# Optimization experiments

Measured on AMD Instinct MI355X. Metric: run time of the kernel, lower is better.

## Reference

```python
import math
import jax, jax.numpy as jnp
import numpy as np

B, C, H, W = 64, 1536, 16, 16
M_CLUSTERS, L_DIM, G_DIM, HID = 64, 128, 256, 512


def setup_inputs() -> dict:
    key = jax.random.key(0)
    ks = jax.random.split(key, 10)

    def w(k, out_d, in_d):
        return jax.random.normal(k, (out_d, in_d), jnp.float32) * (1.0 / np.sqrt(in_d))

    return {
        "x": jax.random.normal(ks[0], (B, C, H, W), jnp.float32),
        "t": jax.random.normal(ks[1], (B, C), jnp.float32),
        # token_features: Linear(C,512) -> ReLU -> Linear(512, token_dim)
        "Wt1": w(ks[2], HID, C), "bt1": jnp.zeros((HID,), jnp.float32),
        "Wt2": w(ks[3], G_DIM, HID), "bt2": jnp.zeros((G_DIM,), jnp.float32),
        # cluster_features: Conv1x1(C,512) -> ReLU -> Conv1x1(512, cluster_dim)
        "Wc1": w(ks[4], HID, C), "bc1": jnp.zeros((HID,), jnp.float32),
        "Wc2": w(ks[5], L_DIM, HID), "bc2": jnp.zeros((L_DIM,), jnp.float32),
        # score: Conv1x1(C,512) -> ReLU -> Conv1x1(512, num_clusters)
        "Ws1": w(ks[6], HID, C), "bs1": jnp.zeros((HID,), jnp.float32),
        "Ws2": w(ks[7], M_CLUSTERS, HID), "bs2": jnp.zeros((M_CLUSTERS,), jnp.float32),
        "dust_bin": jnp.float32(1.0),
    }


def _l2norm(a, axis):
    n = jnp.maximum(jnp.linalg.norm(a, axis=axis, keepdims=True), 1e-12)
    return a / n


def _conv1x1_mlp(xf, W1, b1, W2, b2):
    # xf: [B, C, N]; 1x1 convs are channel GEMMs
    h = jax.nn.relu(jnp.einsum('oc,bcn->bon', W1, xf) + b1[None, :, None])
    return jnp.einsum('oc,bcn->bon', W2, h) + b2[None, :, None]


def _matching_probs(S, dust_bin, num_iters=3):
    # Sinkhorn with dustbin row (log domain), reg = 1.0
    b, m, n = S.shape
    dust_row = jnp.broadcast_to(dust_bin.astype(S.dtype), (b, 1, n))
    Ms = jnp.concatenate([S, dust_row], axis=1)  # [B, m+1, n]
    norm = -math.log(n + m)
    log_a = jnp.full((m + 1,), norm, S.dtype).at[-1].add(math.log(n - m))
    log_b = jnp.full((n,), norm, S.dtype)
    u = jnp.zeros((b, m + 1), S.dtype)
    v = jnp.zeros((b, n), S.dtype)
    for _ in range(num_iters):
        u = log_a[None, :] - jax.scipy.special.logsumexp(Ms + v[:, None, :], axis=2)
        v = log_b[None, :] - jax.scipy.special.logsumexp(Ms + u[:, :, None], axis=1)
    return Ms + u[:, :, None] + v[:, None, :] - norm  # log_P - norm


def reference(x, t, Wt1, bt1, Wt2, bt2, Wc1, bc1, Wc2, bc2, Ws1, bs1, Ws2, bs2, dust_bin):
    b, c, h, w = x.shape
    n = h * w
    xf = x.reshape(b, c, n)
    f = _conv1x1_mlp(xf, Wc1, bc1, Wc2, bc2)      # [B, l, N]
    s = _conv1x1_mlp(xf, Ws1, bs1, Ws2, bs2)      # [B, m, N]
    tok = jax.nn.relu(t @ Wt1.T + bt1) @ Wt2.T + bt2  # [B, g]

    log_p = _matching_probs(s, dust_bin, num_iters=3)
    p = jnp.exp(log_p)[:, :-1, :]                 # drop dustbin row -> [B, m, N]

    # (f.unsqueeze(2) * p.unsqueeze(1)).sum(-1) is exactly a batched matmul
    vlad = jnp.einsum('bln,bmn->blm', f, p)       # [B, l, m]
    vlad = _l2norm(vlad, axis=1).reshape(b, -1)   # intra-norm over l, then flatten(1)

    out = jnp.concatenate([_l2norm(tok, axis=-1), vlad], axis=-1)
    return _l2norm(out, axis=-1)
```

## Files before the change

kernel.cpp:

```cpp
#include <hip/hip_runtime.h>
#include <math.h>

#define BNT 16384

using f32x4 = __attribute__((ext_vector_type(4))) float;
using s16x8 = __attribute__((ext_vector_type(8))) short;

__device__ __forceinline__ unsigned short f32_to_bf16_rne(float f) {
  unsigned int u = __float_as_uint(f);
  u += 0x7FFFu + ((u >> 16) & 1u);
  return (unsigned short)(u >> 16);
}
__device__ __forceinline__ unsigned pack_bf16x2(float a, float b) {
  return (unsigned)f32_to_bf16_rne(a) | ((unsigned)f32_to_bf16_rne(b) << 16);
}

__device__ __forceinline__ void gload_lds16(const ushort* g, ushort* lds) {
  __builtin_amdgcn_global_load_lds(
      (const __attribute__((address_space(1))) unsigned int*)g,
      (__attribute__((address_space(3))) unsigned int*)lds, 16, 0, 0);
}

__global__ __launch_bounds__(256) void prep_all(
    const float* __restrict__ t, const float* __restrict__ Wt1,
    const float* __restrict__ Wt2, const float* __restrict__ Wc1,
    const float* __restrict__ Ws1, const float* __restrict__ bc1,
    const float* __restrict__ bs1, const float* __restrict__ Wc2,
    const float* __restrict__ Ws2, const float* __restrict__ bc2,
    const float* __restrict__ bs2, ushort* __restrict__ Tb,
    ushort* __restrict__ Wt1b, ushort* __restrict__ Wt2b,
    ushort* __restrict__ Wc1b, ushort* __restrict__ Ws1b,
    float* __restrict__ b1, ushort* __restrict__ A2, float* __restrict__ b2) {
  const int bid = blockIdx.x, tid = threadIdx.x;
  const float* src = nullptr;
  ushort* dst = nullptr;
  int i = 0;
  if (bid < 96) {
    src = t; dst = Tb; i = bid * 256 + tid;
  } else if (bid < 864) {
    src = Wt1; dst = Wt1b; i = (bid - 96) * 256 + tid;
  } else if (bid < 992) {
    src = Wt2; dst = Wt2b; i = (bid - 864) * 256 + tid;
  } else if (bid < 1760) {
    src = Wc1; dst = Wc1b; i = (bid - 992) * 256 + tid;
  } else if (bid < 2528) {
    src = Ws1; dst = Ws1b; i = (bid - 1760) * 256 + tid;
  } else if (bid < 2532) {
    const int j = (bid - 2528) * 256 + tid;
    b1[j] = j < 512 ? bc1[j] : bs1[j - 512];
    return;
  } else {
    const int r = bid - 2532;
    const int c = tid * 4;
    float v[4] = {0.f, 0.f, 0.f, 0.f};
    if (r < 128) {
      if (c < 512) {
#pragma unroll
        for (int j = 0; j < 4; ++j) v[j] = Wc2[r * 512 + c + j];
      }
    } else if (r < 192) {
      if (c >= 512) {
#pragma unroll
        for (int j = 0; j < 4; ++j) v[j] = Ws2[(r - 128) * 512 + (c - 512) + j];
      }
    }
    uint2 o;
    o.x = pack_bf16x2(v[0], v[1]);
    o.y = pack_bf16x2(v[2], v[3]);
    *(uint2*)(A2 + r * 1024 + c) = o;
    if (tid == 0) b2[r] = r < 128 ? bc2[r] : (r < 192 ? bs2[r - 128] : 0.f);
    return;
  }
  const float4 v = ((const float4*)src)[i];
  uint2 o;
  o.x = pack_bf16x2(v.x, v.y);
  o.y = pack_bf16x2(v.z, v.w);
  ((uint2*)dst)[i] = o;
}

__global__ __launch_bounds__(256) void token1_mfma(
    const ushort* __restrict__ Tb, const ushort* __restrict__ Wt1b,
    float* __restrict__ Pt) {
  const int ct = blockIdx.x, kc = blockIdx.y;
  const int tid = threadIdx.x, l = tid & 63, wv = tid >> 6;
  const int lr = l & 15, ko = l >> 4;
  const int col = ct * 64 + wv * 16 + lr;
  f32x4 acc[4];
#pragma unroll
  for (int r = 0; r < 4; ++r) acc[r] = (f32x4){0.f, 0.f, 0.f, 0.f};
  const int k0 = kc * 384;
#pragma unroll 4
  for (int ks = 0; ks < 12; ++ks) {
    const int k = k0 + ks * 32 + ko * 8;
    const s16x8 bf = *(const s16x8*)(Wt1b + (size_t)col * 1536 + k);
#pragma unroll
    for (int rf = 0; rf < 4; ++rf) {
      const s16x8 af = *(const s16x8*)(Tb + (size_t)(rf * 16 + lr) * 1536 + k);
      acc[rf] =
          __builtin_amdgcn_mfma_f32_16x16x32_bf16(af, bf, acc[rf], 0, 0, 0);
    }
  }
#pragma unroll
  for (int rf = 0; rf < 4; ++rf)
#pragma unroll
    for (int j = 0; j < 4; ++j) {
      const int row = rf * 16 + ko * 4 + j;
      Pt[((kc * 64 + row) << 9) + col] = acc[rf][j];
    }
}

__global__ __launch_bounds__(256) void token1_reduce(
    const float* __restrict__ Pt, const float* __restrict__ bt1,
    ushort* __restrict__ Hb) {
  const int i = blockIdx.x * 256 + threadIdx.x;
  const int row = i >> 8, c2 = (i & 255) * 2;
  float v0 = bt1[c2], v1 = bt1[c2 + 1];
#pragma unroll
  for (int kc = 0; kc < 4; ++kc) {
    v0 += Pt[((kc * 64 + row) << 9) + c2];
    v1 += Pt[((kc * 64 + row) << 9) + c2 + 1];
  }
  v0 = fmaxf(v0, 0.f);
  v1 = fmaxf(v1, 0.f);
  ((unsigned*)Hb)[i] = pack_bf16x2(v0, v1);
}

__global__ __launch_bounds__(256) void token2_mfma(
    const ushort* __restrict__ Hb, const ushort* __restrict__ Wt2b,
    const float* __restrict__ bt2, float* __restrict__ TK) {
  const int ct = blockIdx.x;
  const int tid = threadIdx.x, l = tid & 63, wv = tid >> 6;
  const int lr = l & 15, ko = l >> 4;
  const int col = ct * 64 + wv * 16 + lr;
  f32x4 acc[4];
#pragma unroll
  for (int r = 0; r < 4; ++r) acc[r] = (f32x4){0.f, 0.f, 0.f, 0.f};
#pragma unroll 4
  for (int ks = 0; ks < 16; ++ks) {
    const int k = ks * 32 + ko * 8;
    const s16x8 bf = *(const s16x8*)(Wt2b + (size_t)col * 512 + k);
#pragma unroll
    for (int rf = 0; rf < 4; ++rf) {
      const s16x8 af = *(const s16x8*)(Hb + (size_t)(rf * 16 + lr) * 512 + k);
      acc[rf] =
          __builtin_amdgcn_mfma_f32_16x16x32_bf16(af, bf, acc[rf], 0, 0, 0);
    }
  }
  const float bb = bt2[col];
#pragma unroll
  for (int rf = 0; rf < 4; ++rf)
#pragma unroll
    for (int j = 0; j < 4; ++j)
      TK[(rf * 16 + ko * 4 + j) * 256 + col] = acc[rf][j] + bb;
}

__global__ __launch_bounds__(256) void transpose_x_bf16(
    const float* __restrict__ x, ushort* __restrict__ XT) {
  __shared__ ushort lds[16384];
  const int cc = blockIdx.x * 64, b = blockIdx.y;
  const int t = threadIdx.x;
  const float* xb = x + b * 393216 + cc * 256;
#pragma unroll
  for (int i = 0; i < 16; ++i) {
    const int c0 = i * 4;
    const float v0 = xb[(c0 + 0) * 256 + t];
    const float v1 = xb[(c0 + 1) * 256 + t];
    const float v2 = xb[(c0 + 2) * 256 + t];
    const float v3 = xb[(c0 + 3) * 256 + t];
    uint2 o;
    o.x = pack_bf16x2(v0, v1);
    o.y = pack_bf16x2(v2, v3);
    const int g = c0 >> 3;
    const int waddr = t * 128 + (((g ^ (t & 7)) << 4) | ((c0 & 7) << 1));
    *(uint2*)((char*)lds + waddr) = o;
  }
  __syncthreads();
#pragma unroll
  for (int r = 0; r < 8; ++r) {
    const int j = r * 32 + (t >> 3), q = t & 7;
    const uint4 o =
        *(const uint4*)((const char*)lds + j * 128 + ((q ^ (j & 7)) << 4));
    *(uint4*)(XT + (size_t)(b * 256 + j) * 1536 + cc + q * 8) = o;
  }
}

__global__ __launch_bounds__(512) void gemm1_8ph(
    const ushort* __restrict__ A1, const ushort* __restrict__ Bt,
    const float* __restrict__ b1, ushort* __restrict__ HT) {
  __shared__ ushort lds[65536];
  const int tid = threadIdx.x, l = tid & 63, w = tid >> 6;
  const int bid = blockIdx.x;
  const int newid = (bid & 7) * 32 + (bid >> 3);
  const int m0 = (newid & 3) * 256, n0 = (newid >> 2) * 256;
  const int wr = w >> 2, wc = w & 3;
  const int lr = l & 15, kq = l >> 4;
  const int permK8 = (kq ^ ((lr >> 1) & 3)) * 8;
  const int aRow = wr * 128 + lr;
  const int bRow = wc * 64 + lr;

  f32x4 acc[8][4];
#pragma unroll
  for (int mi = 0; mi < 8; ++mi)
#pragma unroll
    for (int ni = 0; ni < 4; ++ni) acc[mi][ni] = (f32x4){0.f, 0.f, 0.f, 0.f};

  const int srow = tid >> 2, ssp = tid & 3;
  const int skq = ssp ^ ((srow >> 1) & 3);
  const ushort* sA0 = A1 + (size_t)(m0 + srow) * 1536 + skq * 8;
  const ushort* sA1 = A1 + (size_t)(m0 + srow + 128) * 1536 + skq * 8;
  const ushort* sB0 = Bt + (size_t)(n0 + srow) * 1536 + skq * 8;
  const ushort* sB1 = Bt + (size_t)(n0 + srow + 128) * 1536 + skq * 8;
  const int wofs = w * 512;

#define STG_A(tau, kh)                                              \
  do {                                                              \
    ushort* d = &lds[((((tau)&1) * 2 + (kh)) * 8192) + wofs];       \
    gload_lds16(sA0 + (tau)*64 + (kh)*32, d);                       \
    gload_lds16(sA1 + (tau)*64 + (kh)*32, d + 4096);                \
  } while (0)
#define STG_B(tau, kh)                                              \
  do {                                                              \
    ushort* d = &lds[32768 + ((((tau)&1) * 2 + (kh)) * 8192) + wofs]; \
    gload_lds16(sB0 + (tau)*64 + (kh)*32, d);                       \
    gload_lds16(sB1 + (tau)*64 + (kh)*32, d + 4096);                \
  } while (0)

  STG_A(0, 0);
  STG_B(0, 0);
  STG_A(0, 1);
  STG_B(0, 1);
  asm volatile("s_waitcnt vmcnt(0)" ::: "memory");
  __builtin_amdgcn_s_barrier();

  for (int sg = 0; sg < 24; ++sg) {
    const int rho = sg & 1;
    const int As0 = (rho * 2 + 0) * 8192, As1 = (rho * 2 + 1) * 8192;
    const int Bs0 = 32768 + As0, Bs1 = 32768 + As1;
    const bool st = (sg + 1) < 24;
    s16x8 af[4], bfv[4];

#pragma unroll
    for (int i = 0; i < 4; ++i)
      af[i] = *(const s16x8*)&lds[As0 + (aRow + i * 16) * 32 + permK8];
#pragma unroll
    for (int ni = 0; ni < 4; ++ni)
      bfv[ni] = *(const s16x8*)&lds[Bs0 + (bRow + ni * 16) * 32 + permK8];
    if (st) STG_A(sg + 1, 0);
    __builtin_amdgcn_s_barrier();
    __builtin_amdgcn_s_setprio(1);
#pragma unroll
    for (int i = 0; i < 4; ++i)
#pragma unroll
      for (int ni = 0; ni < 4; ++ni)
        acc[i][ni] = __builtin_amdgcn_mfma_f32_16x16x32_bf16(af[i], bfv[ni],
                                                             acc[i][ni], 0, 0, 0);
    __builtin_amdgcn_s_setprio(0);
    __builtin_amdgcn_s_barrier();

#pragma unroll
    for (int i = 0; i < 4; ++i)
      af[i] = *(const s16x8*)&lds[As0 + (aRow + 64 + i * 16) * 32 + permK8];
    if (st) STG_B(sg + 1, 0);
    if (sg < 23)
      asm volatile("s_waitcnt vmcnt(4)" ::: "memory");
    else
      asm volatile("s_waitcnt vmcnt(0)" ::: "memory");
    __builtin_amdgcn_s_barrier();
    __builtin_amdgcn_s_setprio(1);
#pragma unroll
    for (int i = 0; i < 4; ++i)
#pragma unroll
      for (int ni = 0; ni < 4; ++ni)
        acc[4 + i][ni] = __builtin_amdgcn_mfma_f32_16x16x32_bf16(
            af[i], bfv[ni], acc[4 + i][ni], 0, 0, 0);
    __builtin_amdgcn_s_setprio(0);
    __builtin_amdgcn_s_barrier();

#pragma unroll
    for (int i = 0; i < 4; ++i)
      af[i] = *(const s16x8*)&lds[As1 + (aRow + i * 16) * 32 + permK8];
#pragma unroll
    for (int ni = 0; ni < 4; ++ni)
      bfv[ni] = *(const s16x8*)&lds[Bs1 + (bRow + ni * 16) * 32 + permK8];
    if (st) STG_A(sg + 1, 1);
    __builtin_amdgcn_s_barrier();
    __builtin_amdgcn_s_setprio(1);
#pragma unroll
    for (int i = 0; i < 4; ++i)
#pragma unroll
      for (int ni = 0; ni < 4; ++ni)
        acc[i][ni] = __builtin_amdgcn_mfma_f32_16x16x32_bf16(af[i], bfv[ni],
                                                             acc[i][ni], 0, 0, 0);
    __builtin_amdgcn_s_setprio(0);
    __builtin_amdgcn_s_barrier();

#pragma unroll
    for (int i = 0; i < 4; ++i)
      af[i] = *(const s16x8*)&lds[As1 + (aRow + 64 + i * 16) * 32 + permK8];
    if (st) STG_B(sg + 1, 1);
    asm volatile("s_waitcnt vmcnt(4)" ::: "memory");
    __builtin_amdgcn_s_barrier();
    __builtin_amdgcn_s_setprio(1);
#pragma unroll
    for (int i = 0; i < 4; ++i)
#pragma unroll
      for (int ni = 0; ni < 4; ++ni)
        acc[4 + i][ni] = __builtin_amdgcn_mfma_f32_16x16x32_bf16(
            af[i], bfv[ni], acc[4 + i][ni], 0, 0, 0);
    __builtin_amdgcn_s_setprio(0);
    __builtin_amdgcn_s_barrier();
  }
#undef STG_A
#undef STG_B

#pragma unroll
  for (int mi = 0; mi < 8; ++mi) {
    const int rbase = m0 + wr * 128 + mi * 16 + kq * 4;
    float b4[4];
#pragma unroll
    for (int j = 0; j < 4; ++j) b4[j] = b1[rbase + j];
#pragma unroll
    for (int ni = 0; ni < 4; ++ni) {
      const int col = n0 + wc * 64 + ni * 16 + lr;
      const float v0 = fmaxf(acc[mi][ni][0] + b4[0], 0.f);
      const float v1 = fmaxf(acc[mi][ni][1] + b4[1], 0.f);
      const float v2 = fmaxf(acc[mi][ni][2] + b4[2], 0.f);
      const float v3 = fmaxf(acc[mi][ni][3] + b4[3], 0.f);
      uint2 o;
      o.x = pack_bf16x2(v0, v1);
      o.y = pack_bf16x2(v2, v3);
      *(uint2*)(HT + (size_t)col * 1024 + rbase) = o;
    }
  }
}

__global__ __launch_bounds__(256) void gemm2_mfma(
    const ushort* __restrict__ A2, const ushort* __restrict__ HT,
    const float* __restrict__ b2, float* __restrict__ C2,
    ushort* __restrict__ Fb) {
  constexpr int K = 1024;
  __shared__ ushort As[2 * 128 * 32];
  __shared__ ushort Bs[2 * 128 * 32];
  const int tid = threadIdx.x;
  const int l = tid & 63, w = tid >> 6;
  const int bid = blockIdx.x;
  const int newid = (bid & 7) * 32 + (bid >> 3);
  const int m0 = (newid & 1) * 128, n0 = (newid >> 1) * 128;
  const int wr = w >> 1, wc = w & 1;
  const int lr = l & 15, kq = l >> 4;

  f32x4 acc[4][4];
#pragma unroll
  for (int mi = 0; mi < 4; ++mi)
#pragma unroll
    for (int ni = 0; ni < 4; ++ni) acc[mi][ni] = (f32x4){0.f, 0.f, 0.f, 0.f};

  const int rA0 = tid >> 2;
  const int q8 = (tid & 3) * 8;
  ushort* AsW0 = As + (w * 64) * 8;
  ushort* AsW1 = As + (256 + w * 64) * 8;
  ushort* BsW0 = Bs + (w * 64) * 8;
  ushort* BsW1 = Bs + (256 + w * 64) * 8;
  const ushort* Arow0 = A2 + (size_t)(m0 + rA0) * K + q8;
  const ushort* Arow1 = A2 + (size_t)(m0 + rA0 + 64) * K + q8;
  const ushort* Brow0 = HT + (size_t)(n0 + rA0) * K + q8;
  const ushort* Brow1 = HT + (size_t)(n0 + rA0 + 64) * K + q8;

  gload_lds16(Arow0, AsW0);
  gload_lds16(Arow1, AsW1);
  gload_lds16(Brow0, BsW0);
  gload_lds16(Brow1, BsW1);
  __syncthreads();

  int cur = 0;
  for (int k0 = 0; k0 < K; k0 += 32) {
    const int nxt = cur ^ 1;
    if (k0 + 32 < K) {
      gload_lds16(Arow0 + k0 + 32, AsW0 + nxt * 4096);
      gload_lds16(Arow1 + k0 + 32, AsW1 + nxt * 4096);
      gload_lds16(Brow0 + k0 + 32, BsW0 + nxt * 4096);
      gload_lds16(Brow1 + k0 + 32, BsW1 + nxt * 4096);
    }
    const ushort* Ab = As + cur * 4096;
    const ushort* Bb = Bs + cur * 4096;
    s16x8 af[4], bfr[4];
#pragma unroll
    for (int mi = 0; mi < 4; ++mi)
      af[mi] = *(const s16x8*)(Ab + (wr * 64 + mi * 16 + lr) * 32 + kq * 8);
#pragma unroll
    for (int ni = 0; ni < 4; ++ni)
      bfr[ni] = *(const s16x8*)(Bb + (wc * 64 + ni * 16 + lr) * 32 + kq * 8);
#pragma unroll
    for (int mi = 0; mi < 4; ++mi)
#pragma unroll
      for (int ni = 0; ni < 4; ++ni)
        acc[mi][ni] = __builtin_amdgcn_mfma_f32_16x16x32_bf16(
            af[mi], bfr[ni], acc[mi][ni], 0, 0, 0);
    __syncthreads();
    cur = nxt;
  }

#pragma unroll
  for (int mi = 0; mi < 4; ++mi) {
    const int rbase = m0 + wr * 64 + mi * 16 + kq * 4;
    if (rbase < 192) {
      float b4[4];
#pragma unroll
      for (int j = 0; j < 4; ++j) b4[j] = b2[rbase + j];
      if (rbase < 128) {
#pragma unroll
        for (int ni = 0; ni < 4; ++ni) {
          const int col = n0 + wc * 64 + ni * 16 + lr;
#pragma unroll
          for (int j = 0; j < 4; ++j)
            Fb[(size_t)(rbase + j) * BNT + col] =
                f32_to_bf16_rne(acc[mi][ni][j] + b4[j]);
        }
      } else {
#pragma unroll
        for (int ni = 0; ni < 4; ++ni) {
          const int col = n0 + wc * 64 + ni * 16 + lr;
          float* cr = C2 + (size_t)rbase * BNT + col;
#pragma unroll
          for (int j = 0; j < 4; ++j)
            cr[(size_t)j * BNT] = acc[mi][ni][j] + b4[j];
        }
      }
    }
  }
}

__global__ __launch_bounds__(256) void sinkhorn_lin(
    const float* __restrict__ S, const float* __restrict__ dustp,
    ushort* __restrict__ Pb) {
  const int b = blockIdx.x, tid = threadIdx.x;
  const int lane = tid & 63, wave = tid >> 6;
  __shared__ float E[65][256];
  __shared__ float U[65];
  __shared__ float V[256];
  for (int idx = tid; idx < 16384; idx += 256) {
    const int m = idx >> 8, n = idx & 255;
    E[m][n] = expf(S[m * BNT + b * 256 + n]);
  }
  E[64][tid] = expf(dustp[0]);
  V[tid] = 1.f;
  const float Ai = 1.f / 320.f;
  const float Adust = 192.f / 320.f;
  const float Bn = 1.f / 320.f;
  __syncthreads();
  for (int it = 0; it < 3; ++it) {
    for (int i = wave; i < 65; i += 4) {
      float s = E[i][lane] * V[lane];
      s = fmaf(E[i][lane + 64], V[lane + 64], s);
      s = fmaf(E[i][lane + 128], V[lane + 128], s);
      s = fmaf(E[i][lane + 192], V[lane + 192], s);
#pragma unroll
      for (int off = 32; off; off >>= 1) s += __shfl_xor(s, off);
      if (lane == 0) U[i] = (i == 64 ? Adust : Ai) / s;
    }
    __syncthreads();
    {
      const int n = tid;
      float s = 0.f;
#pragma unroll 13
      for (int i = 0; i < 65; ++i) s = fmaf(E[i][n], U[i], s);
      V[n] = Bn / s;
    }
    __syncthreads();
  }
  for (int idx = tid; idx < 16384; idx += 256) {
    const int m = idx >> 8, n = idx & 255;
    Pb[b * 16384 + idx] = f32_to_bf16_rne(E[m][n] * U[m] * V[n] * 320.f);
  }
}

__global__ __launch_bounds__(256) void vlad_mfma(const ushort* __restrict__ Fb,
                                                 const ushort* __restrict__ Pb,
                                                 float* __restrict__ VL) {
  const int b = blockIdx.x;
  const int tid = threadIdx.x, l = tid & 63, w = tid >> 6;
  const int lr = l & 15, ko = l >> 4;
  f32x4 acc[2][4];
#pragma unroll
  for (int li = 0; li < 2; ++li)
#pragma unroll
    for (int ni = 0; ni < 4; ++ni) acc[li][ni] = (f32x4){0.f, 0.f, 0.f, 0.f};
  const ushort* Fbase = Fb + b * 256;
  const ushort* Pbase = Pb + b * 16384;
#pragma unroll
  for (int ks = 0; ks < 8; ++ks) {
    const int k = ks * 32 + ko * 8;
    s16x8 bfr[4];
#pragma unroll
    for (int ni = 0; ni < 4; ++ni)
      bfr[ni] = *(const s16x8*)(Pbase + (ni * 16 + lr) * 256 + k);
#pragma unroll
    for (int li = 0; li < 2; ++li) {
      const s16x8 af =
          *(const s16x8*)(Fbase + (size_t)(w * 32 + li * 16 + lr) * BNT + k);
#pragma unroll
      for (int ni = 0; ni < 4; ++ni)
        acc[li][ni] = __builtin_amdgcn_mfma_f32_16x16x32_bf16(
            af, bfr[ni], acc[li][ni], 0, 0, 0);
    }
  }
#pragma unroll
  for (int li = 0; li < 2; ++li)
#pragma unroll
    for (int ni = 0; ni < 4; ++ni)
#pragma unroll
      for (int j = 0; j < 4; ++j) {
        const int ll = w * 32 + li * 16 + ko * 4 + j;
        const int m = ni * 16 + lr;
        VL[b * 8192 + ll * 64 + m] = acc[li][ni][j];
      }
}

__global__ __launch_bounds__(256) void finalize_kernel(
    const float* __restrict__ TK, const float* __restrict__ VL,
    float* __restrict__ out) {
  const int b = blockIdx.x, tid = threadIdx.x;
  const int lane = tid & 63, wave = tid >> 6;
  __shared__ float sred[4];
  __shared__ float ssm_part[4][64];
  __shared__ float invm_s[64];
  __shared__ float totals[1];
  const float* vl = &VL[b * 8192];
  float accv = 0.f;
  for (int k = 0; k < 32; ++k) {
    const float xv = vl[tid + 256 * k];
    accv = fmaf(xv, xv, accv);
  }
  ssm_part[wave][lane] = accv;
  const float tv = TK[b * 256 + tid];
  float ss = tv * tv;
#pragma unroll
  for (int off = 32; off; off >>= 1) ss += __shfl_down(ss, off);
  if (lane == 0) sred[wave] = ss;
  __syncthreads();
  const float sstok = sred[0] + sred[1] + sred[2] + sred[3];
  const float invtok = 1.f / fmaxf(sqrtf(sstok), 1e-12f);
  float tpart = 0.f;
  if (wave == 0) {
    const float s4 = ssm_part[0][tid] + ssm_part[1][tid] + ssm_part[2][tid] +
                     ssm_part[3][tid];
    const float inv = 1.f / fmaxf(sqrtf(s4), 1e-12f);
    invm_s[tid] = inv;
    tpart = s4 * inv * inv;
#pragma unroll
    for (int off = 32; off; off >>= 1) tpart += __shfl_down(tpart, off);
    if (lane == 0) totals[0] = tpart;
  }
  __syncthreads();
  const float total = totals[0] + sstok * invtok * invtok;
  const float invT = 1.f / fmaxf(sqrtf(total), 1e-12f);
  float* ob = &out[b * 8448];
  ob[tid] = tv * invtok * invT;
  for (int k = 0; k < 32; ++k) {
    const int idx = tid + 256 * k;
    ob[256 + idx] = vl[idx] * invm_s[idx & 63] * invT;
  }
}

template <bool RELU>
__global__ __launch_bounds__(256) void gemm_tt(
    const float* __restrict__ A, const float* __restrict__ Bw,
    const float* __restrict__ bias, float* __restrict__ C, int K, int Nn) {
  __shared__ float As[16][68];
  __shared__ float Bs[16][68];
  const int tid = threadIdx.x;
  const int tx = tid & 15, ty = tid >> 4;
  const int n0 = blockIdx.x * 64;
  const int lrow = tid >> 2, lkq = (tid & 3) << 2;
  float acc[4][4];
#pragma unroll
  for (int r = 0; r < 4; ++r)
#pragma unroll
    for (int c = 0; c < 4; ++c) acc[r][c] = 0.f;
  for (int k0 = 0; k0 < K; k0 += 16) {
    const float4 av = *(const float4*)&A[lrow * K + k0 + lkq];
    const float4 bv = *(const float4*)&Bw[(n0 + lrow) * K + k0 + lkq];
    As[lkq + 0][lrow] = av.x;
    As[lkq + 1][lrow] = av.y;
    As[lkq + 2][lrow] = av.z;
    As[lkq + 3][lrow] = av.w;
    Bs[lkq + 0][lrow] = bv.x;
    Bs[lkq + 1][lrow] = bv.y;
    Bs[lkq + 2][lrow] = bv.z;
    Bs[lkq + 3][lrow] = bv.w;
    __syncthreads();
#pragma unroll
    for (int kk = 0; kk < 16; ++kk) {
      const float4 a4 = *(const float4*)&As[kk][ty << 2];
      const float4 b4 = *(const float4*)&Bs[kk][tx << 2];
      acc[0][0] = fmaf(a4.x, b4.x, acc[0][0]);
      acc[0][1] = fmaf(a4.x, b4.y, acc[0][1]);
      acc[0][2] = fmaf(a4.x, b4.z, acc[0][2]);
      acc[0][3] = fmaf(a4.x, b4.w, acc[0][3]);
      acc[1][0] = fmaf(a4.y, b4.x, acc[1][0]);
      acc[1][1] = fmaf(a4.y, b4.y, acc[1][1]);
      acc[1][2] = fmaf(a4.y, b4.z, acc[1][2]);
      acc[1][3] = fmaf(a4.y, b4.w, acc[1][3]);
      acc[2][0] = fmaf(a4.z, b4.x, acc[2][0]);
      acc[2][1] = fmaf(a4.z, b4.y, acc[2][1]);
      acc[2][2] = fmaf(a4.z, b4.z, acc[2][2]);
      acc[2][3] = fmaf(a4.z, b4.w, acc[2][3]);
      acc[3][0] = fmaf(a4.w, b4.x, acc[3][0]);
      acc[3][1] = fmaf(a4.w, b4.y, acc[3][1]);
      acc[3][2] = fmaf(a4.w, b4.z, acc[3][2]);
      acc[3][3] = fmaf(a4.w, b4.w, acc[3][3]);
    }
    __syncthreads();
  }
#pragma unroll
  for (int r = 0; r < 4; ++r) {
    const int row = (ty << 2) + r;
    float4 o;
    o.x = acc[r][0] + bias[n0 + (tx << 2) + 0];
    o.y = acc[r][1] + bias[n0 + (tx << 2) + 1];
    o.z = acc[r][2] + bias[n0 + (tx << 2) + 2];
    o.w = acc[r][3] + bias[n0 + (tx << 2) + 3];
    if (RELU) {
      o.x = fmaxf(o.x, 0.f);
      o.y = fmaxf(o.y, 0.f);
      o.z = fmaxf(o.z, 0.f);
      o.w = fmaxf(o.w, 0.f);
    }
    *(float4*)&C[row * Nn + n0 + (tx << 2)] = o;
  }
}

template <bool XVIEW, bool RELU>
__global__ __launch_bounds__(256) void gemm_tile(
    const float* __restrict__ A, const float* __restrict__ Bsrc,
    const float* __restrict__ bias, float* __restrict__ Cout, int K) {
  __shared__ float As[16][68];
  __shared__ float Bsh[16][68];
  const int tid = threadIdx.x;
  const int tx = tid & 15, ty = tid >> 4;
  const int rowBase = blockIdx.y * 64;
  const int colBase = blockIdx.x * 64;
  const int bb = colBase >> 8, n0 = colBase & 255;
  const int boff = XVIEW ? (bb * 393216 + n0) : colBase;
  const int la_row = tid >> 2, la_kq = (tid & 3) << 2;
  const int lb_k = tid >> 4, lb_c = (tid & 15) << 2;
  float acc[4][4];
#pragma unroll
  for (int r = 0; r < 4; ++r)
#pragma unroll
    for (int c = 0; c < 4; ++c) acc[r][c] = 0.f;
  for (int k0 = 0; k0 < K; k0 += 16) {
    const float4 av = *(const float4*)&A[(rowBase + la_row) * K + k0 + la_kq];
    float4 bv;
    if (XVIEW)
      bv = *(const float4*)&Bsrc[boff + (k0 + lb_k) * 256 + lb_c];
    else
      bv = *(const float4*)&Bsrc[(k0 + lb_k) * BNT + boff + lb_c];
    As[la_kq + 0][la_row] = av.x;
    As[la_kq + 1][la_row] = av.y;
    As[la_kq + 2][la_row] = av.z;
    As[la_kq + 3][la_row] = av.w;
    *(float4*)&Bsh[lb_k][lb_c] = bv;
    __syncthreads();
#pragma unroll
    for (int kk = 0; kk < 16; ++kk) {
      const float4 a4 = *(const float4*)&As[kk][ty << 2];
      const float4 b4 = *(const float4*)&Bsh[kk][tx << 2];
      acc[0][0] = fmaf(a4.x, b4.x, acc[0][0]);
      acc[0][1] = fmaf(a4.x, b4.y, acc[0][1]);
      acc[0][2] = fmaf(a4.x, b4.z, acc[0][2]);
      acc[0][3] = fmaf(a4.x, b4.w, acc[0][3]);
      acc[1][0] = fmaf(a4.y, b4.x, acc[1][0]);
      acc[1][1] = fmaf(a4.y, b4.y, acc[1][1]);
      acc[1][2] = fmaf(a4.y, b4.z, acc[1][2]);
      acc[1][3] = fmaf(a4.y, b4.w, acc[1][3]);
      acc[2][0] = fmaf(a4.z, b4.x, acc[2][0]);
      acc[2][1] = fmaf(a4.z, b4.y, acc[2][1]);
      acc[2][2] = fmaf(a4.z, b4.z, acc[2][2]);
      acc[2][3] = fmaf(a4.z, b4.w, acc[2][3]);
      acc[3][0] = fmaf(a4.w, b4.x, acc[3][0]);
      acc[3][1] = fmaf(a4.w, b4.y, acc[3][1]);
      acc[3][2] = fmaf(a4.w, b4.z, acc[3][2]);
      acc[3][3] = fmaf(a4.w, b4.w, acc[3][3]);
    }
    __syncthreads();
  }
#pragma unroll
  for (int r = 0; r < 4; ++r) {
    const int row = rowBase + (ty << 2) + r;
    const float bsv = bias[row];
    float4 o;
    o.x = acc[r][0] + bsv;
    o.y = acc[r][1] + bsv;
    o.z = acc[r][2] + bsv;
    o.w = acc[r][3] + bsv;
    if (RELU) {
      o.x = fmaxf(o.x, 0.f);
      o.y = fmaxf(o.y, 0.f);
      o.z = fmaxf(o.z, 0.f);
      o.w = fmaxf(o.w, 0.f);
    }
    *(float4*)&Cout[row * BNT + colBase + (tx << 2)] = o;
  }
}

__global__ __launch_bounds__(256) void sinkhorn_kernel(
    const float* __restrict__ S, const float* __restrict__ dustp,
    float* __restrict__ P) {
  const int b = blockIdx.x, tid = threadIdx.x;
  const int lane = tid & 63, wave = tid >> 6;
  __shared__ float Ms[65][256];
  __shared__ float u[65];
  __shared__ float v[256];
  const float dust = dustp[0];
  for (int idx = tid; idx < 16384; idx += 256) {
    const int m = idx >> 8, n = idx & 255;
    Ms[m][n] = S[m * BNT + b * 256 + n];
  }
  Ms[64][tid] = dust;
  v[tid] = 0.f;
  if (tid < 65) u[tid] = 0.f;
  const float norm = -logf(320.f);
  const float la_dust = norm + logf(192.f);
  __syncthreads();
  for (int it = 0; it < 3; ++it) {
    for (int i = wave; i < 65; i += 4) {
      const float x0 = Ms[i][lane] + v[lane];
      const float x1 = Ms[i][lane + 64] + v[lane + 64];
      const float x2 = Ms[i][lane + 128] + v[lane + 128];
      const float x3 = Ms[i][lane + 192] + v[lane + 192];
      float mm = fmaxf(fmaxf(x0, x1), fmaxf(x2, x3));
#pragma unroll
      for (int off = 32; off; off >>= 1) mm = fmaxf(mm, __shfl_xor(mm, off));
      float s = expf(x0 - mm) + expf(x1 - mm) + expf(x2 - mm) + expf(x3 - mm);
#pragma unroll
      for (int off = 32; off; off >>= 1) s += __shfl_xor(s, off);
      if (lane == 0) u[i] = (i == 64 ? la_dust : norm) - (logf(s) + mm);
    }
    __syncthreads();
    {
      const int n = tid;
      float mm = -1e30f;
      for (int i = 0; i < 65; ++i) mm = fmaxf(mm, Ms[i][n] + u[i]);
      float s = 0.f;
      for (int i = 0; i < 65; ++i) s += expf(Ms[i][n] + u[i] - mm);
      v[n] = norm - (logf(s) + mm);
    }
    __syncthreads();
  }
  for (int idx = tid; idx < 16384; idx += 256) {
    const int m = idx >> 8, n = idx & 255;
    P[b * 16384 + idx] = expf(Ms[m][n] + u[m] + v[n] - norm);
  }
}

__device__ __forceinline__ int ps_idx(int m, int n) {
  return m * 256 + ((((n >> 2) ^ (m & 7)) << 2) | (n & 3));
}
__global__ __launch_bounds__(256) void vlad_kernel(const float* __restrict__ F,
                                                   const float* __restrict__ P,
                                                   float* __restrict__ VL) {
  const int b = blockIdx.x, half = blockIdx.y;
  const int tid = threadIdx.x;
  const int m = tid & 63, lg = tid >> 6;
  __shared__ float ps[64 * 256];
  for (int idx = tid; idx < 16384; idx += 256) {
    const int mm = idx >> 8, n = idx & 255;
    ps[ps_idx(mm, n)] = P[b * 16384 + idx];
  }
  __syncthreads();
  float acc[16];
#pragma unroll
  for (int i = 0; i < 16; ++i) acc[i] = 0.f;
  for (int i = 0; i < 16; ++i) {
    const int ll = half * 64 + lg + 4 * i;
    const float* frow = &F[(size_t)ll * BNT + b * 256];
    float a = 0.f;
#pragma unroll 8
    for (int nq = 0; nq < 64; ++nq) {
      const float4 f4 = *(const float4*)&frow[nq << 2];
      const float4 p4 = *(const float4*)&ps[m * 256 + ((nq ^ (m & 7)) << 2)];
      a = fmaf(f4.x, p4.x, a);
      a = fmaf(f4.y, p4.y, a);
      a = fmaf(f4.z, p4.z, a);
      a = fmaf(f4.w, p4.w, a);
    }
    acc[i] = a;
  }
#pragma unroll
  for (int i = 0; i < 16; ++i) {
    const int ll = half * 64 + lg + 4 * i;
    VL[b * 8192 + ll * 64 + m] = acc[i];
  }
}

extern "C" void kernel_launch(void* const* d_in, const int* in_sizes, int n_in,
                              void* d_out, int out_size, void* d_ws,
                              size_t ws_size, hipStream_t stream) {
  const float* x = (const float*)d_in[0];
  const float* t = (const float*)d_in[1];
  const float* Wt1 = (const float*)d_in[2];
  const float* bt1 = (const float*)d_in[3];
  const float* Wt2 = (const float*)d_in[4];
  const float* bt2 = (const float*)d_in[5];
  const float* Wc1 = (const float*)d_in[6];
  const float* bc1 = (const float*)d_in[7];
  const float* Wc2 = (const float*)d_in[8];
  const float* bc2 = (const float*)d_in[9];
  const float* Ws1 = (const float*)d_in[10];
  const float* bs1 = (const float*)d_in[11];
  const float* Ws2 = (const float*)d_in[12];
  const float* bs2 = (const float*)d_in[13];
  const float* dust = (const float*)d_in[14];
  float* out = (float*)d_out;

  if (ws_size >= 97714176ull) {
    char* base = (char*)d_ws;
    ushort* Tb = (ushort*)base;
    ushort* Wt1b = (ushort*)(base + 196608);
    ushort* Wt2b = (ushort*)(base + 1769472);
    float* Pt = (float*)(base + 2031616);
    ushort* Hb = (ushort*)(base + 2555904);
    ushort* XT = (ushort*)base;
    ushort* Pb = (ushort*)base;
    float* VL = (float*)(base + 4194304);
    ushort* Fb = (ushort*)(base + 8388608);
    ushort* HT = (ushort*)(base + 50331648);
    float* C2 = (float*)(base + 83886080);
    ushort* A1 = (ushort*)(base + 83886080);
    ushort* Wc1b = A1;
    ushort* Ws1b = (ushort*)(base + 85458944);
    ushort* A2 = (ushort*)(base + 96468992);
    float* b2 = (float*)(base + 96993280);
    float* TK = (float*)(base + 96994304);
    float* b1 = (float*)(base + 97059840);
    float* Sb = C2 + (size_t)128 * BNT;

    prep_all<<<2788, 256, 0, stream>>>(t, Wt1, Wt2, Wc1, Ws1, bc1, bs1, Wc2,
                                       Ws2, bc2, bs2, Tb, Wt1b, Wt2b, Wc1b,
                                       Ws1b, b1, A2, b2);
    token1_mfma<<<dim3(8, 4), 256, 0, stream>>>(Tb, Wt1b, Pt);
    token1_reduce<<<64, 256, 0, stream>>>(Pt, bt1, Hb);
    token2_mfma<<<4, 256, 0, stream>>>(Hb, Wt2b, bt2, TK);
    transpose_x_bf16<<<dim3(24, 64), 256, 0, stream>>>(x, XT);
    gemm1_8ph<<<256, 512, 0, stream>>>(A1, XT, b1, HT);
    gemm2_mfma<<<256, 256, 0, stream>>>(A2, HT, b2, C2, Fb);
    sinkhorn_lin<<<64, 256, 0, stream>>>(Sb, dust, Pb);
    vlad_mfma<<<64, 256, 0, stream>>>(Fb, Pb, VL);
    finalize_kernel<<<64, 256, 0, stream>>>(TK, VL, out);
  } else {
    float* ws = (float*)d_ws;
    float* H = ws;
    float* F = H + 512 * BNT;
    float* Sb = F + 128 * BNT;
    float* P = Sb + 64 * BNT;
    float* VL = P + 64 * BNT;
    float* TK = VL + 64 * 8192;
    float* Hh = P;

    gemm_tt<true><<<dim3(8, 1), 256, 0, stream>>>(t, Wt1, bt1, Hh, 1536, 512);
    gemm_tt<false><<<dim3(4, 1), 256, 0, stream>>>(Hh, Wt2, bt2, TK, 512, 256);
    gemm_tile<true, true><<<dim3(256, 8), 256, 0, stream>>>(Wc1, x, bc1, H, 1536);
    gemm_tile<false, false><<<dim3(256, 2), 256, 0, stream>>>(Wc2, H, bc2, F, 512);
    gemm_tile<true, true><<<dim3(256, 8), 256, 0, stream>>>(Ws1, x, bs1, H, 1536);
    gemm_tile<false, false><<<dim3(256, 1), 256, 0, stream>>>(Ws2, H, bs2, Sb, 512);
    sinkhorn_kernel<<<64, 256, 0, stream>>>(Sb, dust, P);
    vlad_kernel<<<dim3(64, 2), 256, 0, stream>>>(F, P, VL);
    finalize_kernel<<<64, 256, 0, stream>>>(TK, VL, out);
  }
}
```

Before: 169.2 us.

## Cut gemm1 phase barriers and shrink gemm2 M-tile to the 192 valid rows

The first big GEMM drops the per-phase barriers, s_setprio hints and staged vmcnt waits, keeping one vmcnt(0) wait and one barrier per double-buffer iteration. This removes synchronisation overhead but gives up fine-grained load and MFMA interleaving and priority scheduling. The second GEMM moves from 128-row to 96-row M tiles, so its two M-blocks cover exactly the 192 real output rows. That removes the wasted MFMA work and loads on padded rows 192-255, at the cost of an uneven A-tile load (only half the threads issue the second A load).

```diff
diff --git a/kernel.cpp b/kernel.cpp
--- a/kernel.cpp
+++ b/kernel.cpp
@@ -184,7 +184,7 @@
   }
 }
 
-__global__ __launch_bounds__(512) void gemm1_8ph(
+__global__ __launch_bounds__(512) void gemm1_win(
     const ushort* __restrict__ A1, const ushort* __restrict__ Bt,
     const float* __restrict__ b1, ushort* __restrict__ HT) {
   __shared__ ushort lds[65536];
@@ -246,35 +246,23 @@
     for (int ni = 0; ni < 4; ++ni)
       bfv[ni] = *(const s16x8*)&lds[Bs0 + (bRow + ni * 16) * 32 + permK8];
     if (st) STG_A(sg + 1, 0);
-    __builtin_amdgcn_s_barrier();
-    __builtin_amdgcn_s_setprio(1);
 #pragma unroll
     for (int i = 0; i < 4; ++i)
 #pragma unroll
       for (int ni = 0; ni < 4; ++ni)
         acc[i][ni] = __builtin_amdgcn_mfma_f32_16x16x32_bf16(af[i], bfv[ni],
                                                              acc[i][ni], 0, 0, 0);
-    __builtin_amdgcn_s_setprio(0);
-    __builtin_amdgcn_s_barrier();
 
 #pragma unroll
     for (int i = 0; i < 4; ++i)
       af[i] = *(const s16x8*)&lds[As0 + (aRow + 64 + i * 16) * 32 + permK8];
     if (st) STG_B(sg + 1, 0);
-    if (sg < 23)
-      asm volatile("s_waitcnt vmcnt(4)" ::: "memory");
-    else
-      asm volatile("s_waitcnt vmcnt(0)" ::: "memory");
-    __builtin_amdgcn_s_barrier();
-    __builtin_amdgcn_s_setprio(1);
 #pragma unroll
     for (int i = 0; i < 4; ++i)
 #pragma unroll
       for (int ni = 0; ni < 4; ++ni)
         acc[4 + i][ni] = __builtin_amdgcn_mfma_f32_16x16x32_bf16(
             af[i], bfv[ni], acc[4 + i][ni], 0, 0, 0);
-    __builtin_amdgcn_s_setprio(0);
-    __builtin_amdgcn_s_barrier();
 
 #pragma unroll
     for (int i = 0; i < 4; ++i)
@@ -283,31 +271,25 @@
     for (int ni = 0; ni < 4; ++ni)
       bfv[ni] = *(const s16x8*)&lds[Bs1 + (bRow + ni * 16) * 32 + permK8];
     if (st) STG_A(sg + 1, 1);
-    __builtin_amdgcn_s_barrier();
-    __builtin_amdgcn_s_setprio(1);
 #pragma unroll
     for (int i = 0; i < 4; ++i)
 #pragma unroll
       for (int ni = 0; ni < 4; ++ni)
         acc[i][ni] = __builtin_amdgcn_mfma_f32_16x16x32_bf16(af[i], bfv[ni],
                                                              acc[i][ni], 0, 0, 0);
-    __builtin_amdgcn_s_setprio(0);
-    __builtin_amdgcn_s_barrier();
 
 #pragma unroll
     for (int i = 0; i < 4; ++i)
       af[i] = *(const s16x8*)&lds[As1 + (aRow + 64 + i * 16) * 32 + permK8];
     if (st) STG_B(sg + 1, 1);
-    asm volatile("s_waitcnt vmcnt(4)" ::: "memory");
-    __builtin_amdgcn_s_barrier();
-    __builtin_amdgcn_s_setprio(1);
 #pragma unroll
     for (int i = 0; i < 4; ++i)
 #pragma unroll
       for (int ni = 0; ni < 4; ++ni)
         acc[4 + i][ni] = __builtin_amdgcn_mfma_f32_16x16x32_bf16(
             af[i], bfv[ni], acc[4 + i][ni], 0, 0, 0);
-    __builtin_amdgcn_s_setprio(0);
+
+    if (st) asm volatile("s_waitcnt vmcnt(0)" ::: "memory");
     __builtin_amdgcn_s_barrier();
   }
 #undef STG_A
@@ -334,64 +316,62 @@
   }
 }
 
-__global__ __launch_bounds__(256) void gemm2_mfma(
+__global__ __launch_bounds__(256) void gemm2_mfma96(
     const ushort* __restrict__ A2, const ushort* __restrict__ HT,
     const float* __restrict__ b2, float* __restrict__ C2,
     ushort* __restrict__ Fb) {
   constexpr int K = 1024;
-  __shared__ ushort As[2 * 128 * 32];
-  __shared__ ushort Bs[2 * 128 * 32];
+  __shared__ ushort As[2 * 3072];
+  __shared__ ushort Bs[2 * 4096];
   const int tid = threadIdx.x;
   const int l = tid & 63, w = tid >> 6;
   const int bid = blockIdx.x;
   const int newid = (bid & 7) * 32 + (bid >> 3);
-  const int m0 = (newid & 1) * 128, n0 = (newid >> 1) * 128;
+  const int m0 = (newid & 1) * 96, n0 = (newid >> 1) * 128;
   const int wr = w >> 1, wc = w & 1;
   const int lr = l & 15, kq = l >> 4;
 
-  f32x4 acc[4][4];
-#pragma unroll
-  for (int mi = 0; mi < 4; ++mi)
+  f32x4 acc[3][4];
+#pragma unroll
+  for (int mi = 0; mi < 3; ++mi)
 #pragma unroll
     for (int ni = 0; ni < 4; ++ni) acc[mi][ni] = (f32x4){0.f, 0.f, 0.f, 0.f};
 
-  const int rA0 = tid >> 2;
+  const int srow = tid >> 2;
   const int q8 = (tid & 3) * 8;
-  ushort* AsW0 = As + (w * 64) * 8;
-  ushort* AsW1 = As + (256 + w * 64) * 8;
-  ushort* BsW0 = Bs + (w * 64) * 8;
-  ushort* BsW1 = Bs + (256 + w * 64) * 8;
-  const ushort* Arow0 = A2 + (size_t)(m0 + rA0) * K + q8;
-  const ushort* Arow1 = A2 + (size_t)(m0 + rA0 + 64) * K + q8;
-  const ushort* Brow0 = HT + (size_t)(n0 + rA0) * K + q8;
-  const ushort* Brow1 = HT + (size_t)(n0 + rA0 + 64) * K + q8;
-
-  gload_lds16(Arow0, AsW0);
-  gload_lds16(Arow1, AsW1);
-  gload_lds16(Brow0, BsW0);
-  gload_lds16(Brow1, BsW1);
+  const bool secondA = tid < 128;
+  const ushort* sA0 = A2 + (size_t)(m0 + srow) * K + q8;
+  const ushort* sA1 = A2 + (size_t)(m0 + srow + 64) * K + q8;
+  const ushort* sB0 = HT + (size_t)(n0 + srow) * K + q8;
+  const ushort* sB1 = HT + (size_t)(n0 + srow + 64) * K + q8;
+  const int wofs = w * 512;
+
+#define STAGE2(k0v, buf)                                            \
+  do {                                                              \
+    gload_lds16(sA0 + (k0v), As + (buf)*3072 + wofs);               \
+    if (secondA) gload_lds16(sA1 + (k0v), As + (buf)*3072 + 2048 + wofs); \
+    gload_lds16(sB0 + (k0v), Bs + (buf)*4096 + wofs);               \
+    gload_lds16(sB1 + (k0v), Bs + (buf)*4096 + 2048 + wofs);        \
+  } while (0)
+
+  STAGE2(0, 0);
   __syncthreads();
 
   int cur = 0;
   for (int k0 = 0; k0 < K; k0 += 32) {
     const int nxt = cur ^ 1;
-    if (k0 + 32 < K) {
-      gload_lds16(Arow0 + k0 + 32, AsW0 + nxt * 4096);
-      gload_lds16(Arow1 + k0 + 32, AsW1 + nxt * 4096);
-      gload_lds16(Brow0 + k0 + 32, BsW0 + nxt * 4096);
-      gload_lds16(Brow1 + k0 + 32, BsW1 + nxt * 4096);
-    }
-    const ushort* Ab = As + cur * 4096;
+    if (k0 + 32 < K) STAGE2(k0 + 32, nxt);
+    const ushort* Ab = As + cur * 3072;
     const ushort* Bb = Bs + cur * 4096;
-    s16x8 af[4], bfr[4];
-#pragma unroll
-    for (int mi = 0; mi < 4; ++mi)
-      af[mi] = *(const s16x8*)(Ab + (wr * 64 + mi * 16 + lr) * 32 + kq * 8);
+    s16x8 af[3], bfr[4];
+#pragma unroll
+    for (int mi = 0; mi < 3; ++mi)
+      af[mi] = *(const s16x8*)(Ab + (wr * 48 + mi * 16 + lr) * 32 + kq * 8);
 #pragma unroll
     for (int ni = 0; ni < 4; ++ni)
       bfr[ni] = *(const s16x8*)(Bb + (wc * 64 + ni * 16 + lr) * 32 + kq * 8);
 #pragma unroll
-    for (int mi = 0; mi < 4; ++mi)
+    for (int mi = 0; mi < 3; ++mi)
 #pragma unroll
       for (int ni = 0; ni < 4; ++ni)
         acc[mi][ni] = __builtin_amdgcn_mfma_f32_16x16x32_bf16(
@@ -399,32 +379,30 @@
     __syncthreads();
     cur = nxt;
   }
-
-#pragma unroll
-  for (int mi = 0; mi < 4; ++mi) {
-    const int rbase = m0 + wr * 64 + mi * 16 + kq * 4;
-    if (rbase < 192) {
-      float b4[4];
-#pragma unroll
-      for (int j = 0; j < 4; ++j) b4[j] = b2[rbase + j];
-      if (rbase < 128) {
-#pragma unroll
-        for (int ni = 0; ni < 4; ++ni) {
-          const int col = n0 + wc * 64 + ni * 16 + lr;
-#pragma unroll
-          for (int j = 0; j < 4; ++j)
-            Fb[(size_t)(rbase + j) * BNT + col] =
-                f32_to_bf16_rne(acc[mi][ni][j] + b4[j]);
-        }
-      } else {
-#pragma unroll
-        for (int ni = 0; ni < 4; ++ni) {
-          const int col = n0 + wc * 64 + ni * 16 + lr;
-          float* cr = C2 + (size_t)rbase * BNT + col;
-#pragma unroll
-          for (int j = 0; j < 4; ++j)
-            cr[(size_t)j * BNT] = acc[mi][ni][j] + b4[j];
-        }
+#undef STAGE2
+
+#pragma unroll
+  for (int mi = 0; mi < 3; ++mi) {
+    const int rbase = m0 + wr * 48 + mi * 16 + kq * 4;
+    float b4[4];
+#pragma unroll
+    for (int j = 0; j < 4; ++j) b4[j] = b2[rbase + j];
+    if (rbase < 128) {
+#pragma unroll
+      for (int ni = 0; ni < 4; ++ni) {
+        const int col = n0 + wc * 64 + ni * 16 + lr;
+#pragma unroll
+        for (int j = 0; j < 4; ++j)
+          Fb[(size_t)(rbase + j) * BNT + col] =
+              f32_to_bf16_rne(acc[mi][ni][j] + b4[j]);
+      }
+    } else {
+#pragma unroll
+      for (int ni = 0; ni < 4; ++ni) {
+        const int col = n0 + wc * 64 + ni * 16 + lr;
+        float* cr = C2 + (size_t)rbase * BNT + col;
+#pragma unroll
+        for (int j = 0; j < 4; ++j) cr[(size_t)j * BNT] = acc[mi][ni][j] + b4[j];
       }
     }
   }
@@ -843,8 +821,8 @@
     token1_reduce<<<64, 256, 0, stream>>>(Pt, bt1, Hb);
     token2_mfma<<<4, 256, 0, stream>>>(Hb, Wt2b, bt2, TK);
     transpose_x_bf16<<<dim3(24, 64), 256, 0, stream>>>(x, XT);
-    gemm1_8ph<<<256, 512, 0, stream>>>(A1, XT, b1, HT);
-    gemm2_mfma<<<256, 256, 0, stream>>>(A2, HT, b2, C2, Fb);
+    gemm1_win<<<256, 512, 0, stream>>>(A1, XT, b1, HT);
+    gemm2_mfma96<<<256, 256, 0, stream>>>(A2, HT, b2, C2, Fb);
     sinkhorn_lin<<<64, 256, 0, stream>>>(Sb, dust, Pb);
     vlad_mfma<<<64, 256, 0, stream>>>(Fb, Pb, VL);
     finalize_kernel<<<64, 256, 0, stream>>>(TK, VL, out);
```

Result: no change. 166.1 us (-1.8%).
